# Kernel tuning notes

Measured on AMD Instinct MI355X. Metric: run time of the kernel, lower is better.

The kernel has to match this reference:

```python
import jax, jax.numpy as jnp
import numpy as np

N = 20000
E = 320000
F_IN = 256
NHID = 64
H1 = 8
H2 = 1
NUM_CLASSES = 40
NEG_SLOPE = 0.2


def setup_inputs() -> dict:
    key = jax.random.key(0)
    ks = jax.random.split(key, 11)
    glorot = lambda k, shape: jax.random.normal(k, shape, jnp.float32) * jnp.sqrt(2.0 / (shape[0] + shape[-1]))
    x = jax.random.normal(ks[0], (N, F_IN), jnp.float32)
    edge_index = jax.random.randint(ks[1], (2, E), 0, N, jnp.int64)
    W1 = glorot(ks[2], (F_IN, H1 * NHID))
    att_src1 = glorot(ks[3], (H1, NHID))
    att_dst1 = glorot(ks[4], (H1, NHID))
    b1 = jnp.zeros((H1 * NHID,), jnp.float32)
    W2 = glorot(ks[5], (H1 * NHID, H2 * NUM_CLASSES))
    att_src2 = glorot(ks[6], (H2, NUM_CLASSES))
    att_dst2 = glorot(ks[7], (H2, NUM_CLASSES))
    b2 = jnp.zeros((NUM_CLASSES,), jnp.float32)
    return {"x": x, "edge_index": edge_index, "W1": W1, "att_src1": att_src1,
            "att_dst1": att_dst1, "b1": b1, "W2": W2, "att_src2": att_src2,
            "att_dst2": att_dst2, "b2": b2}


def gat_conv(x, src, dst, W, a_src, a_dst, bias, concat):
    # x: [N, F_in], src/dst: [E'] (self-loops already appended)
    H, C = a_src.shape
    h = (x @ W).reshape(N, H, C)                       # [N,H,C]
    alpha_src = jnp.sum(h * a_src, axis=-1)            # [N,H]
    alpha_dst = jnp.sum(h * a_dst, axis=-1)            # [N,H]
    e = jax.nn.leaky_relu(alpha_src[src] + alpha_dst[dst], NEG_SLOPE)  # [E',H]
    # segment softmax over incoming edges of each dst node
    emax = jax.lax.stop_gradient(jax.ops.segment_max(e, dst, num_segments=N))
    ee = jnp.exp(e - emax[dst])
    denom = jax.ops.segment_sum(ee, dst, num_segments=N)
    alpha = ee / (denom[dst] + 1e-16)                  # [E',H]
    out = jax.ops.segment_sum(alpha[:, :, None] * h[src], dst, num_segments=N)  # [N,H,C]
    out = out.reshape(N, H * C) if concat else out.mean(axis=1)
    return out + bias


def reference(x, edge_index, W1, att_src1, att_dst1, b1, W2, att_src2, att_dst2, b2):
    # PyG GATConv adds self-loops by default
    loops = jnp.arange(N, dtype=edge_index.dtype)
    src = jnp.concatenate([edge_index[0], loops])
    dst = jnp.concatenate([edge_index[1], loops])
    h = gat_conv(x, src, dst, W1, att_src1, att_dst1, b1, concat=True)   # [N, H1*NHID]
    h = jax.nn.elu(h)
    out = gat_conv(h, src, dst, W2, att_src2, att_dst2, b2, concat=False)  # [N, NUM_CLASSES]
    return jax.nn.log_softmax(out, axis=1)
```

## Files before the change

kernel.cpp:

```cpp
#include <hip/hip_runtime.h>
#include <hip/hip_bf16.h>
#include <math.h>

#define N_NODES 20000
#define MPAD 20096
#define N_EDGES 320000
#define EP (N_EDGES + N_NODES)
#define F_IN 256
#define NHID 64
#define H1 8
#define D1 512
#define NCLS 40
#define NEG_SLOPE 0.2f
#define MAXD 128

typedef __attribute__((ext_vector_type(8))) short bf16x8;
typedef __attribute__((ext_vector_type(4))) float f32x4;

__device__ __forceinline__ float wave_max(float v) {
#pragma unroll
  for (int o = 32; o > 0; o >>= 1) v = fmaxf(v, __shfl_xor(v, o));
  return v;
}
__device__ __forceinline__ float wave_sum(float v) {
#pragma unroll
  for (int o = 32; o > 0; o >>= 1) v += __shfl_xor(v, o);
  return v;
}
__device__ __forceinline__ float bf2f(unsigned short u) {
  union { unsigned int i; float f; } c; c.i = ((unsigned int)u) << 16; return c.f;
}
__device__ __forceinline__ unsigned short f2bf(float f) {
  union { float f; unsigned int i; } c; c.f = f;
  unsigned int x = c.i;
  return (unsigned short)((x + 0x7fffu + ((x >> 16) & 1u)) >> 16);
}
__device__ __forceinline__ float asf(unsigned int u) {
  union { unsigned int i; float f; } c; c.i = u; return c.f;
}
__device__ __forceinline__ float lrelu(float x) { return x > 0.f ? x : NEG_SLOPE * x; }

__device__ __forceinline__ void gload16(const void* g, void* l) {
  __builtin_amdgcn_global_load_lds((const __attribute__((address_space(1))) void*)g,
                                   (__attribute__((address_space(3))) void*)l, 16, 0, 0);
}

#define PB_CONV 2512
#define PB_TW1  (PB_CONV + 32)
#define PB_TW2  (PB_TW1 + 96)
#define PB_ZERO (PB_TW2 + 157)
#define PB_PAD  (PB_ZERO + 24)
__global__ __launch_bounds__(256) void prep_kernel(const float* __restrict__ x,
                                                   const float* __restrict__ W1,
                                                   const float* __restrict__ W2,
                                                   unsigned short* __restrict__ xb,
                                                   unsigned short* __restrict__ wb1t,
                                                   unsigned short* __restrict__ wb2t,
                                                   int* __restrict__ deg,
                                                   int* __restrict__ cursor,
                                                   unsigned short* __restrict__ out1b) {
  __shared__ float tsh[64][65];
  int bid = blockIdx.x;
  int t = threadIdx.x;
  if (bid < PB_CONV) {
    size_t base = ((size_t)bid * 256 + t) * 8;
    int row = (int)(base >> 8);
    ushort4 o0, o1;
    if (row < N_NODES) {
      float4 v0 = *(const float4*)&x[base];
      float4 v1 = *(const float4*)&x[base + 4];
      o0 = make_ushort4(f2bf(v0.x), f2bf(v0.y), f2bf(v0.z), f2bf(v0.w));
      o1 = make_ushort4(f2bf(v1.x), f2bf(v1.y), f2bf(v1.z), f2bf(v1.w));
    } else {
      o0 = make_ushort4(0, 0, 0, 0); o1 = o0;
    }
    *(ushort4*)&xb[base] = o0;
    *(ushort4*)&xb[base + 4] = o1;
  } else if (bid < PB_TW1) {
    int b2 = bid - PB_CONV;
    int bk = b2 & 3, bn = b2 >> 2;
    int tr = t >> 4, tc4 = (t & 15) * 4;
#pragma unroll
    for (int i = 0; i < 4; ++i) {
      int k = i * 16 + tr;
      float4 v = *(const float4*)&W1[(size_t)(bk * 64 + k) * D1 + bn * 64 + tc4];
      tsh[k][tc4] = v.x; tsh[k][tc4 + 1] = v.y; tsh[k][tc4 + 2] = v.z; tsh[k][tc4 + 3] = v.w;
    }
    __syncthreads();
#pragma unroll
    for (int i = 0; i < 4; ++i) {
      int n = i * 16 + tr;
      ushort4 o = make_ushort4(f2bf(tsh[tc4][n]), f2bf(tsh[tc4 + 1][n]),
                               f2bf(tsh[tc4 + 2][n]), f2bf(tsh[tc4 + 3][n]));
      *(ushort4*)&wb1t[(size_t)(bn * 64 + n) * F_IN + bk * 64 + tc4] = o;
    }
  } else if (bid < PB_TW2) {
    int idx = (bid - PB_TW1) * 256 + t;
    int c = idx >> 9, k = idx & 511;
    wb2t[idx] = f2bf((c < NCLS) ? W2[(size_t)k * NCLS + c] : 0.f);
  } else if (bid < PB_ZERO) {
    int idx = (bid - PB_TW2) * 256 + t;
    if (idx < N_NODES) deg[idx] = 0;
    else if (idx < 2 * N_NODES) cursor[idx - N_NODES] = 0;
  } else {
    int idx = (bid - PB_ZERO) * 256 + t;
    uint4 z = make_uint4(0, 0, 0, 0);
    *(uint4*)((char*)out1b + (size_t)N_NODES * D1 * 2 + (size_t)idx * 16) = z;
  }
}

__global__ void count_deg(const int* __restrict__ ei, int* __restrict__ deg) {
  int e = blockIdx.x * blockDim.x + threadIdx.x;
  if (e >= EP) return;
  int dst = (e < N_EDGES) ? ei[N_EDGES + e] : (e - N_EDGES);
  atomicAdd(&deg[dst], 1);
}

#define SCAN_T 1024
#define SCAN_CHUNK 20
__global__ __launch_bounds__(1024) void scan_kernel(const int* __restrict__ deg,
                                                    int* __restrict__ offsets) {
  __shared__ int wsum[16];
  int t = threadIdx.x;
  int w = t >> 6, lane = t & 63;
  int lo = t * SCAN_CHUNK;
  int hi = min(lo + SCAN_CHUNK, N_NODES);
  int s = 0;
  for (int i = lo; i < hi; ++i) s += deg[i];
  int incl = s;
#pragma unroll
  for (int o = 1; o < 64; o <<= 1) {
    int v = __shfl_up(incl, o);
    if (lane >= o) incl += v;
  }
  if (lane == 63) wsum[w] = incl;
  __syncthreads();
  if (t == 0) {
    int run = 0;
#pragma unroll
    for (int i = 0; i < 16; ++i) { int v = wsum[i]; wsum[i] = run; run += v; }
  }
  __syncthreads();
  int off = wsum[w] + incl - s;
  for (int i = lo; i < hi; ++i) { offsets[i] = off; off += deg[i]; }
  if (hi == N_NODES && lo < N_NODES) offsets[N_NODES] = off;
}

__global__ void scatter_edges(const int* __restrict__ ei, const int* __restrict__ offsets,
                              int* __restrict__ cursor, int* __restrict__ edge_src) {
  int e = blockIdx.x * blockDim.x + threadIdx.x;
  if (e >= EP) return;
  int src, dst;
  if (e < N_EDGES) { src = ei[e]; dst = ei[N_EDGES + e]; }
  else             { src = dst = e - N_EDGES; }
  int pos = offsets[dst] + atomicAdd(&cursor[dst], 1);
  edge_src[pos] = src;
}

__global__ __launch_bounds__(256) void gemm1_mfma(const unsigned short* __restrict__ xb,
                                                  const unsigned short* __restrict__ wb1t,
                                                  const float* __restrict__ a_src,
                                                  const float* __restrict__ a_dst,
                                                  unsigned short* __restrict__ h1b,
                                                  float* __restrict__ asrc,
                                                  float* __restrict__ adst) {
  __shared__ unsigned short As[128 * 64];
  __shared__ unsigned short Bs[128 * 64];
  int tid = threadIdx.x;
  int w = tid >> 6, lane = tid & 63;
  int bn = blockIdx.x & 3, bm = blockIdx.x >> 2;
  int row0 = bm * 128, col0 = bn * 128;
  int wr = w >> 1, wc = w & 1;
  int cl = lane & 15, hi = lane >> 4;
  f32x4 acc[4][4] = {};
  for (int k0 = 0; k0 < F_IN; k0 += 64) {
#pragma unroll
    for (int c = 0; c < 4; ++c) {
      int slot = c * 256 + tid;
      int r = slot >> 3;
      int q = (slot & 7) ^ (r & 7);
      gload16(xb + (size_t)(row0 + r) * F_IN + k0 + q * 8, (char*)As + (c * 256 + w * 64) * 16);
      gload16(wb1t + (size_t)(col0 + r) * F_IN + k0 + q * 8, (char*)Bs + (c * 256 + w * 64) * 16);
    }
    __syncthreads();
#pragma unroll
    for (int kk = 0; kk < 2; ++kk) {
      bf16x8 a[4], b[4];
#pragma unroll
      for (int m = 0; m < 4; ++m) {
        int r = wr * 64 + m * 16 + cl;
        a[m] = *(const bf16x8*)&As[r * 64 + ((((kk * 4 + hi)) ^ (r & 7)) << 3)];
      }
#pragma unroll
      for (int n = 0; n < 4; ++n) {
        int r = wc * 64 + n * 16 + cl;
        b[n] = *(const bf16x8*)&Bs[r * 64 + ((((kk * 4 + hi)) ^ (r & 7)) << 3)];
      }
#pragma unroll
      for (int m = 0; m < 4; ++m)
#pragma unroll
        for (int n = 0; n < 4; ++n)
          acc[m][n] = __builtin_amdgcn_mfma_f32_16x16x32_bf16(a[m], b[n], acc[m][n], 0, 0, 0);
    }
    __syncthreads();
  }
  int head = bn * 2 + wc;
  float asv[4], adv[4];
#pragma unroll
  for (int n = 0; n < 4; ++n) {
    asv[n] = a_src[head * 64 + n * 16 + cl];
    adv[n] = a_dst[head * 64 + n * 16 + cl];
  }
#pragma unroll
  for (int m = 0; m < 4; ++m) {
#pragma unroll
    for (int r = 0; r < 4; ++r) {
      int grow = row0 + wr * 64 + m * 16 + hi * 4 + r;
      float ps = acc[m][0][r] * asv[0] + acc[m][1][r] * asv[1] +
                 acc[m][2][r] * asv[2] + acc[m][3][r] * asv[3];
      float pd = acc[m][0][r] * adv[0] + acc[m][1][r] * adv[1] +
                 acc[m][2][r] * adv[2] + acc[m][3][r] * adv[3];
#pragma unroll
      for (int o = 8; o > 0; o >>= 1) { ps += __shfl_xor(ps, o); pd += __shfl_xor(pd, o); }
      if (grow < N_NODES) {
#pragma unroll
        for (int n = 0; n < 4; ++n)
          h1b[(size_t)grow * D1 + col0 + wc * 64 + n * 16 + cl] = f2bf(acc[m][n][r]);
        if (cl == 0) { asrc[grow * H1 + head] = ps; adst[grow * H1 + head] = pd; }
      }
    }
  }
}

__global__ __launch_bounds__(128) void agg1_kernel(const int* __restrict__ offsets,
                                                   const int* __restrict__ edge_src,
                                                   const float* __restrict__ asrc,
                                                   const float* __restrict__ adst,
                                                   const unsigned short* __restrict__ h1b,
                                                   const float* __restrict__ b1,
                                                   unsigned short* __restrict__ out1b) {
  __shared__ float alphaT[MAXD][H1 + 1];
  __shared__ int   lsoff[MAXD];
  __shared__ float red[2][8];
  __shared__ float minv[2][8];
  __shared__ float accs[2][D1];
  int n = blockIdx.x;
  int t = threadIdx.x;
  int w = t >> 6, lane = t & 63;
  int base = offsets[n];
  int deg = offsets[n + 1] - base;
  int degc = min(deg, MAXD);

  for (int e = t; e < degc; e += 128) lsoff[e] = edge_src[base + e] << 10;
  __syncthreads();

  int h = t & 7;
  int et = t >> 3;
  float advv = adst[n * H1 + h];
  float m = -INFINITY;
  for (int e = et; e < degc; e += 16) {
    int s = lsoff[e] >> 10;
    float ev = lrelu(asrc[s * H1 + h] + advv);
    alphaT[e][h] = ev;
    m = fmaxf(m, ev);
  }
  for (int e = MAXD + et; e < deg; e += 16)
    m = fmaxf(m, lrelu(asrc[edge_src[base + e] * H1 + h] + advv));
  m = fmaxf(m, __shfl_xor(m, 8));
  m = fmaxf(m, __shfl_xor(m, 16));
  m = fmaxf(m, __shfl_xor(m, 32));
  if (lane < 8) red[w][lane] = m;
  __syncthreads();
  m = fmaxf(red[0][h], red[1][h]);
  float ss = 0.f;
  for (int e = et; e < degc; e += 16) ss += __expf(alphaT[e][h] - m);
  for (int e = MAXD + et; e < deg; e += 16)
    ss += __expf(lrelu(asrc[edge_src[base + e] * H1 + h] + advv) - m);
  ss += __shfl_xor(ss, 8);
  ss += __shfl_xor(ss, 16);
  ss += __shfl_xor(ss, 32);
  __syncthreads();
  if (lane < 8) red[w][lane] = ss;
  __syncthreads();
  float inv = 1.f / (red[0][h] + red[1][h] + 1e-16f);
  if (t < 8) { minv[0][t] = m; minv[1][t] = inv; }
  for (int e = et; e < degc; e += 16)
    alphaT[e][h] = __expf(alphaT[e][h] - m) * inv;
  __syncthreads();

  int myh = lane >> 3;
  const char* hb = (const char*)h1b + lane * 16;
  float acc[8] = {};
  int e = w;
  for (; e + 2 < degc; e += 4) {
    float a0 = alphaT[e][myh];
    float a1 = alphaT[e + 2][myh];
    uint4 u0 = *(const uint4*)(hb + lsoff[e]);
    uint4 u1 = *(const uint4*)(hb + lsoff[e + 2]);
#pragma unroll
    for (int j = 0; j < 4; ++j) {
      unsigned int x0 = ((const unsigned int*)&u0)[j];
      unsigned int x1 = ((const unsigned int*)&u1)[j];
      acc[2 * j]     += a0 * asf(x0 << 16);
      acc[2 * j + 1] += a0 * asf(x0 & 0xffff0000u);
      acc[2 * j]     += a1 * asf(x1 << 16);
      acc[2 * j + 1] += a1 * asf(x1 & 0xffff0000u);
    }
  }
  for (; e < degc; e += 2) {
    float a = alphaT[e][myh];
    uint4 uv = *(const uint4*)(hb + lsoff[e]);
#pragma unroll
    for (int j = 0; j < 4; ++j) {
      unsigned int u = ((const unsigned int*)&uv)[j];
      acc[2 * j]     += a * asf(u << 16);
      acc[2 * j + 1] += a * asf(u & 0xffff0000u);
    }
  }
  if (deg > MAXD) {
    float mh = minv[0][myh], invh = minv[1][myh];
    float advh = adst[n * H1 + myh];
    for (int e2 = MAXD + w; e2 < deg; e2 += 2) {
      int s = edge_src[base + e2];
      float a = __expf(lrelu(asrc[s * H1 + myh] + advh) - mh) * invh;
      uint4 uv = *(const uint4*)(hb + ((size_t)s << 10));
#pragma unroll
      for (int j = 0; j < 4; ++j) {
        unsigned int u = ((const unsigned int*)&uv)[j];
        acc[2 * j]     += a * asf(u << 16);
        acc[2 * j + 1] += a * asf(u & 0xffff0000u);
      }
    }
  }
  *(float4*)&accs[w][lane * 8]     = make_float4(acc[0], acc[1], acc[2], acc[3]);
  *(float4*)&accs[w][lane * 8 + 4] = make_float4(acc[4], acc[5], acc[6], acc[7]);
  __syncthreads();

  int c0 = t * 4;
  float4 s0 = *(float4*)&accs[0][c0];
  float4 s1 = *(float4*)&accs[1][c0];
  float4 bv = *(const float4*)&b1[c0];
  float v0 = s0.x + s1.x + bv.x, v1 = s0.y + s1.y + bv.y;
  float v2 = s0.z + s1.z + bv.z, v3 = s0.w + s1.w + bv.w;
  v0 = v0 > 0.f ? v0 : (__expf(v0) - 1.f);
  v1 = v1 > 0.f ? v1 : (__expf(v1) - 1.f);
  v2 = v2 > 0.f ? v2 : (__expf(v2) - 1.f);
  v3 = v3 > 0.f ? v3 : (__expf(v3) - 1.f);
  ushort4 o = make_ushort4(f2bf(v0), f2bf(v1), f2bf(v2), f2bf(v3));
  *(ushort4*)&out1b[(size_t)n * D1 + c0] = o;
}

__global__ __launch_bounds__(256) void gemm2_mfma(const unsigned short* __restrict__ ab,
                                                  const unsigned short* __restrict__ wb2t,
                                                  const float* __restrict__ a_src2,
                                                  const float* __restrict__ a_dst2,
                                                  float* __restrict__ h2,
                                                  float* __restrict__ asrc,
                                                  float* __restrict__ adst) {
  __shared__ unsigned short As[64 * 64];
  __shared__ unsigned short Bs[48 * 64];
  int tid = threadIdx.x;
  int w = tid >> 6, lane = tid & 63;
  int row0 = blockIdx.x * 64;
  int cl = lane & 15, hi = lane >> 4;
  f32x4 acc[3] = {};
  for (int k0 = 0; k0 < D1; k0 += 64) {
#pragma unroll
    for (int c = 0; c < 2; ++c) {
      int slot = c * 256 + tid;
      int r = slot >> 3;
      int q = (slot & 7) ^ (r & 7);
      gload16(ab + (size_t)(row0 + r) * D1 + k0 + q * 8, (char*)As + (c * 256 + w * 64) * 16);
    }
    {
      int r = tid >> 3;
      int q = (tid & 7) ^ (r & 7);
      gload16(wb2t + (size_t)r * D1 + k0 + q * 8, (char*)Bs + (w * 64) * 16);
      if (tid < 128) {
        int slot2 = 256 + tid;
        int r2 = slot2 >> 3;
        int q2 = (slot2 & 7) ^ (r2 & 7);
        gload16(wb2t + (size_t)r2 * D1 + k0 + q2 * 8, (char*)Bs + ((256 + w * 64)) * 16);
      }
    }
    __syncthreads();
#pragma unroll
    for (int kk = 0; kk < 2; ++kk) {
      int ra = w * 16 + cl;
      bf16x8 a = *(const bf16x8*)&As[ra * 64 + (((kk * 4 + hi) ^ (ra & 7)) << 3)];
#pragma unroll
      for (int n = 0; n < 3; ++n) {
        int rb = n * 16 + cl;
        bf16x8 b = *(const bf16x8*)&Bs[rb * 64 + (((kk * 4 + hi) ^ (rb & 7)) << 3)];
        acc[n] = __builtin_amdgcn_mfma_f32_16x16x32_bf16(a, b, acc[n], 0, 0, 0);
      }
    }
    __syncthreads();
  }
  float asv[3], adv[3];
#pragma unroll
  for (int n = 0; n < 3; ++n) {
    int c = n * 16 + cl;
    asv[n] = (c < NCLS) ? a_src2[c] : 0.f;
    adv[n] = (c < NCLS) ? a_dst2[c] : 0.f;
  }
#pragma unroll
  for (int r = 0; r < 4; ++r) {
    int grow = row0 + w * 16 + hi * 4 + r;
    float ps = acc[0][r] * asv[0] + acc[1][r] * asv[1] + acc[2][r] * asv[2];
    float pd = acc[0][r] * adv[0] + acc[1][r] * adv[1] + acc[2][r] * adv[2];
#pragma unroll
    for (int o = 8; o > 0; o >>= 1) { ps += __shfl_xor(ps, o); pd += __shfl_xor(pd, o); }
    if (grow < N_NODES) {
#pragma unroll
      for (int n = 0; n < 3; ++n) {
        int c = n * 16 + cl;
        if (c < NCLS) h2[(size_t)grow * NCLS + c] = acc[n][r];
      }
      if (cl == 0) { asrc[grow] = ps; adst[grow] = pd; }
    }
  }
}

__global__ __launch_bounds__(256) void agg2_kernel(const int* __restrict__ offsets,
                                                   const int* __restrict__ edge_src,
                                                   const float* __restrict__ asrc,
                                                   const float* __restrict__ adst,
                                                   const float* __restrict__ h2,
                                                   const float* __restrict__ b2,
                                                   float* __restrict__ out) {
  __shared__ float lalpha[4][MAXD];
  __shared__ int   lsoff[4][MAXD];
  int w = threadIdx.x >> 6;
  int lane = threadIdx.x & 63;
  int n = blockIdx.x * 4 + w;
  int base = offsets[n];
  int deg = offsets[n + 1] - base;
  int degc = min(deg, MAXD);
  int degp = ((degc + 2) / 3) * 3;

  float advv = adst[n];
  float m = -INFINITY;
  for (int e = lane; e < deg; e += 64) {
    int s = edge_src[base + e];
    float ev = lrelu(asrc[s] + advv);
    if (e < MAXD) { lsoff[w][e] = s * (NCLS * 4); lalpha[w][e] = ev; }
    m = fmaxf(m, ev);
  }
  m = wave_max(m);
  float ssum = 0.f;
  for (int e = lane; e < deg; e += 64) {
    float ev;
    if (e < MAXD) ev = lalpha[w][e];
    else { int s = edge_src[base + e]; ev = lrelu(asrc[s] + advv); }
    ssum += __expf(ev - m);
  }
  float inv = 1.f / (wave_sum(ssum) + 1e-16f);
  for (int e = lane; e < degc; e += 64) lalpha[w][e] = __expf(lalpha[w][e] - m) * inv;
  {
    int e = degc + lane;
    if (e < degp && e < MAXD) { lalpha[w][e] = 0.f; lsoff[w][e] = 0; }
  }

  int esub = lane / 20;
  int cg = lane - esub * 20;
  bool act = esub < 3;
  float ax = 0.f, ay = 0.f;
  const char* hb = (const char*)h2 + cg * 8;
  for (int i = 0; i < degp; i += 3) {
    if (act) {
      int slot = i + esub;
      float a = lalpha[w][slot];
      int so = lsoff[w][slot];
      float2 hv = *(const float2*)(hb + so);
      ax += a * hv.x; ay += a * hv.y;
    }
  }
  for (int e = MAXD + esub; e < deg; e += 3) {
    if (act) {
      int s = edge_src[base + e];
      float a = __expf(lrelu(asrc[s] + advv) - m) * inv;
      float2 hv = *(const float2*)(hb + (size_t)s * (NCLS * 4));
      ax += a * hv.x; ay += a * hv.y;
    }
  }
  float ax1 = __shfl(ax, lane + 20), ax2 = __shfl(ax, lane + 40);
  float ay1 = __shfl(ay, lane + 20), ay2 = __shfl(ay, lane + 40);
  float v0 = -INFINITY, v1 = -INFINITY;
  if (lane < 20) {
    v0 = ax + ax1 + ax2 + b2[2 * cg];
    v1 = ay + ay1 + ay2 + b2[2 * cg + 1];
  }
  float m2 = wave_max(fmaxf(v0, v1));
  float se = wave_sum(lane < 20 ? __expf(v0 - m2) + __expf(v1 - m2) : 0.f);
  if (lane < 20) {
    float ls = logf(se);
    *(float2*)&out[(size_t)n * NCLS + 2 * cg] = make_float2(v0 - m2 - ls, v1 - m2 - ls);
  }
}

extern "C" void kernel_launch(void* const* d_in, const int* in_sizes, int n_in,
                              void* d_out, int out_size, void* d_ws, size_t ws_size,
                              hipStream_t stream) {
  const float* x   = (const float*)d_in[0];
  const int*   ei  = (const int*)d_in[1];
  const float* W1  = (const float*)d_in[2];
  const float* as1 = (const float*)d_in[3];
  const float* ad1 = (const float*)d_in[4];
  const float* b1  = (const float*)d_in[5];
  const float* W2  = (const float*)d_in[6];
  const float* as2 = (const float*)d_in[7];
  const float* ad2 = (const float*)d_in[8];
  const float* b2  = (const float*)d_in[9];
  float* out = (float*)d_out;

  char* ws = (char*)d_ws;
  size_t off = 0;
  auto alloc = [&](size_t bytes) -> char* {
    char* p = ws + off;
    off += (bytes + 255) & ~(size_t)255;
    return p;
  };
  int* deg      = (int*)alloc((size_t)N_NODES * 4);
  int* cursor   = (int*)alloc((size_t)N_NODES * 4);
  int* offsets  = (int*)alloc((size_t)(N_NODES + 1) * 4);
  int* edge_src = (int*)alloc((size_t)EP * 4);
  unsigned short* xb    = (unsigned short*)alloc((size_t)MPAD * F_IN * 2);
  unsigned short* wb1t  = (unsigned short*)alloc((size_t)D1 * F_IN * 2);
  unsigned short* wb2t  = (unsigned short*)alloc((size_t)48 * D1 * 2);
  unsigned short* h1b   = (unsigned short*)alloc((size_t)N_NODES * D1 * 2);
  unsigned short* out1b = (unsigned short*)alloc((size_t)MPAD * D1 * 2);
  float* asrc1  = (float*)alloc((size_t)N_NODES * H1 * 4);
  float* adst1  = (float*)alloc((size_t)N_NODES * H1 * 4);
  float* h2     = (float*)alloc((size_t)N_NODES * NCLS * 4);
  float* asrc2  = (float*)alloc((size_t)N_NODES * 4);
  float* adst2  = (float*)alloc((size_t)N_NODES * 4);

  prep_kernel<<<PB_PAD, 256, 0, stream>>>(x, W1, W2, xb, wb1t, wb2t, deg, cursor, out1b);
  count_deg<<<(EP + 255) / 256, 256, 0, stream>>>(ei, deg);
  scan_kernel<<<1, SCAN_T, 0, stream>>>(deg, offsets);
  scatter_edges<<<(EP + 255) / 256, 256, 0, stream>>>(ei, offsets, cursor, edge_src);

  gemm1_mfma<<<157 * 4, 256, 0, stream>>>(xb, wb1t, as1, ad1, h1b, asrc1, adst1);
  agg1_kernel<<<N_NODES, 128, 0, stream>>>(offsets, edge_src, asrc1, adst1, h1b, b1, out1b);

  gemm2_mfma<<<MPAD / 64, 256, 0, stream>>>(out1b, wb2t, as2, ad2, h2, asrc2, adst2);
  agg2_kernel<<<N_NODES / 4, 256, 0, stream>>>(offsets, edge_src, asrc2, adst2, h2, b2, out);
}
```

Baseline: 159.3 us.

## Map one wavefront per destination node in layer-1 aggregation

The layer-1 aggregation kernel now runs four nodes per 256-thread block, one wavefront each, instead of one node per 128-thread block split across two waves. Block-level barriers and shared-memory reductions are replaced with wave barriers and shuffles, and the final cross-wave accumulator sum through LDS is gone. The intent is to remove synchronisation and reduction overhead and launch fewer blocks. In exchange, each wave walks the full edge list alone, so per-node latency rises and high-degree nodes may cause imbalance within a block. A wave barrier is also added in the layer-2 aggregation kernel.

```diff
diff --git a/kernel.cpp b/kernel.cpp
--- a/kernel.cpp
+++ b/kernel.cpp
@@ -232,71 +232,59 @@
   }
 }
 
-__global__ __launch_bounds__(128) void agg1_kernel(const int* __restrict__ offsets,
+__global__ __launch_bounds__(256) void agg1_kernel(const int* __restrict__ offsets,
                                                    const int* __restrict__ edge_src,
                                                    const float* __restrict__ asrc,
                                                    const float* __restrict__ adst,
                                                    const unsigned short* __restrict__ h1b,
                                                    const float* __restrict__ b1,
                                                    unsigned short* __restrict__ out1b) {
-  __shared__ float alphaT[MAXD][H1 + 1];
-  __shared__ int   lsoff[MAXD];
-  __shared__ float red[2][8];
-  __shared__ float minv[2][8];
-  __shared__ float accs[2][D1];
-  int n = blockIdx.x;
-  int t = threadIdx.x;
-  int w = t >> 6, lane = t & 63;
+  __shared__ float alphaT[4][MAXD][H1];
+  __shared__ int   lsoff[4][MAXD];
+  int w = threadIdx.x >> 6, lane = threadIdx.x & 63;
+  int n = blockIdx.x * 4 + w;
   int base = offsets[n];
   int deg = offsets[n + 1] - base;
   int degc = min(deg, MAXD);
 
-  for (int e = t; e < degc; e += 128) lsoff[e] = edge_src[base + e] << 10;
-  __syncthreads();
-
-  int h = t & 7;
-  int et = t >> 3;
+  for (int e = lane; e < degc; e += 64) lsoff[w][e] = edge_src[base + e] << 10;
+  __builtin_amdgcn_wave_barrier();
+
+  int h = lane & 7, et = lane >> 3;
   float advv = adst[n * H1 + h];
   float m = -INFINITY;
-  for (int e = et; e < degc; e += 16) {
-    int s = lsoff[e] >> 10;
+  for (int e = et; e < degc; e += 8) {
+    int s = lsoff[w][e] >> 10;
     float ev = lrelu(asrc[s * H1 + h] + advv);
-    alphaT[e][h] = ev;
+    alphaT[w][e][h] = ev;
     m = fmaxf(m, ev);
   }
-  for (int e = MAXD + et; e < deg; e += 16)
+  for (int e = MAXD + et; e < deg; e += 8)
     m = fmaxf(m, lrelu(asrc[edge_src[base + e] * H1 + h] + advv));
   m = fmaxf(m, __shfl_xor(m, 8));
   m = fmaxf(m, __shfl_xor(m, 16));
   m = fmaxf(m, __shfl_xor(m, 32));
-  if (lane < 8) red[w][lane] = m;
-  __syncthreads();
-  m = fmaxf(red[0][h], red[1][h]);
   float ss = 0.f;
-  for (int e = et; e < degc; e += 16) ss += __expf(alphaT[e][h] - m);
-  for (int e = MAXD + et; e < deg; e += 16)
+  for (int e = et; e < degc; e += 8) ss += __expf(alphaT[w][e][h] - m);
+  for (int e = MAXD + et; e < deg; e += 8)
     ss += __expf(lrelu(asrc[edge_src[base + e] * H1 + h] + advv) - m);
   ss += __shfl_xor(ss, 8);
   ss += __shfl_xor(ss, 16);
   ss += __shfl_xor(ss, 32);
-  __syncthreads();
-  if (lane < 8) red[w][lane] = ss;
-  __syncthreads();
-  float inv = 1.f / (red[0][h] + red[1][h] + 1e-16f);
-  if (t < 8) { minv[0][t] = m; minv[1][t] = inv; }
-  for (int e = et; e < degc; e += 16)
-    alphaT[e][h] = __expf(alphaT[e][h] - m) * inv;
-  __syncthreads();
+  float inv = 1.f / (ss + 1e-16f);
+  for (int e = et; e < degc; e += 8)
+    alphaT[w][e][h] = __expf(alphaT[w][e][h] - m) * inv;
+  __builtin_amdgcn_wave_barrier();
 
   int myh = lane >> 3;
   const char* hb = (const char*)h1b + lane * 16;
   float acc[8] = {};
-  int e = w;
-  for (; e + 2 < degc; e += 4) {
-    float a0 = alphaT[e][myh];
-    float a1 = alphaT[e + 2][myh];
-    uint4 u0 = *(const uint4*)(hb + lsoff[e]);
-    uint4 u1 = *(const uint4*)(hb + lsoff[e + 2]);
+  int e = 0;
+  for (; e + 1 < degc; e += 2) {
+    float a0 = alphaT[w][e][myh];
+    float a1 = alphaT[w][e + 1][myh];
+    uint4 u0 = *(const uint4*)(hb + lsoff[w][e]);
+    uint4 u1 = *(const uint4*)(hb + lsoff[w][e + 1]);
 #pragma unroll
     for (int j = 0; j < 4; ++j) {
       unsigned int x0 = ((const unsigned int*)&u0)[j];
@@ -307,9 +295,9 @@
       acc[2 * j + 1] += a1 * asf(x1 & 0xffff0000u);
     }
   }
-  for (; e < degc; e += 2) {
-    float a = alphaT[e][myh];
-    uint4 uv = *(const uint4*)(hb + lsoff[e]);
+  for (; e < degc; ++e) {
+    float a = alphaT[w][e][myh];
+    uint4 uv = *(const uint4*)(hb + lsoff[w][e]);
 #pragma unroll
     for (int j = 0; j < 4; ++j) {
       unsigned int u = ((const unsigned int*)&uv)[j];
@@ -318,9 +306,10 @@
     }
   }
   if (deg > MAXD) {
-    float mh = minv[0][myh], invh = minv[1][myh];
+    float mh = __shfl(m, myh);
+    float invh = __shfl(inv, myh);
     float advh = adst[n * H1 + myh];
-    for (int e2 = MAXD + w; e2 < deg; e2 += 2) {
+    for (int e2 = MAXD; e2 < deg; ++e2) {
       int s = edge_src[base + e2];
       float a = __expf(lrelu(asrc[s * H1 + myh] + advh) - mh) * invh;
       uint4 uv = *(const uint4*)(hb + ((size_t)s << 10));
@@ -332,22 +321,19 @@
       }
     }
   }
-  *(float4*)&accs[w][lane * 8]     = make_float4(acc[0], acc[1], acc[2], acc[3]);
-  *(float4*)&accs[w][lane * 8 + 4] = make_float4(acc[4], acc[5], acc[6], acc[7]);
-  __syncthreads();
-
-  int c0 = t * 4;
-  float4 s0 = *(float4*)&accs[0][c0];
-  float4 s1 = *(float4*)&accs[1][c0];
-  float4 bv = *(const float4*)&b1[c0];
-  float v0 = s0.x + s1.x + bv.x, v1 = s0.y + s1.y + bv.y;
-  float v2 = s0.z + s1.z + bv.z, v3 = s0.w + s1.w + bv.w;
-  v0 = v0 > 0.f ? v0 : (__expf(v0) - 1.f);
-  v1 = v1 > 0.f ? v1 : (__expf(v1) - 1.f);
-  v2 = v2 > 0.f ? v2 : (__expf(v2) - 1.f);
-  v3 = v3 > 0.f ? v3 : (__expf(v3) - 1.f);
-  ushort4 o = make_ushort4(f2bf(v0), f2bf(v1), f2bf(v2), f2bf(v3));
-  *(ushort4*)&out1b[(size_t)n * D1 + c0] = o;
+
+  int c0 = lane * 8;
+  float4 b0 = *(const float4*)&b1[c0];
+  float4 b4 = *(const float4*)&b1[c0 + 4];
+  float v[8];
+  v[0] = acc[0] + b0.x; v[1] = acc[1] + b0.y; v[2] = acc[2] + b0.z; v[3] = acc[3] + b0.w;
+  v[4] = acc[4] + b4.x; v[5] = acc[5] + b4.y; v[6] = acc[6] + b4.z; v[7] = acc[7] + b4.w;
+#pragma unroll
+  for (int j = 0; j < 8; ++j) v[j] = v[j] > 0.f ? v[j] : (__expf(v[j]) - 1.f);
+  ushort4 o0 = make_ushort4(f2bf(v[0]), f2bf(v[1]), f2bf(v[2]), f2bf(v[3]));
+  ushort4 o1 = make_ushort4(f2bf(v[4]), f2bf(v[5]), f2bf(v[6]), f2bf(v[7]));
+  *(ushort4*)&out1b[(size_t)n * D1 + c0] = o0;
+  *(ushort4*)&out1b[(size_t)n * D1 + c0 + 4] = o1;
 }
 
 __global__ __launch_bounds__(256) void gemm2_mfma(const unsigned short* __restrict__ ab,
@@ -461,6 +447,7 @@
     int e = degc + lane;
     if (e < degp && e < MAXD) { lalpha[w][e] = 0.f; lsoff[w][e] = 0; }
   }
+  __builtin_amdgcn_wave_barrier();
 
   int esub = lane / 20;
   int cg = lane - esub * 20;
@@ -542,7 +529,7 @@
   scatter_edges<<<(EP + 255) / 256, 256, 0, stream>>>(ei, offsets, cursor, edge_src);
 
   gemm1_mfma<<<157 * 4, 256, 0, stream>>>(xb, wb1t, as1, ad1, h1b, asrc1, adst1);
-  agg1_kernel<<<N_NODES, 128, 0, stream>>>(offsets, edge_src, asrc1, adst1, h1b, b1, out1b);
+  agg1_kernel<<<N_NODES / 4, 256, 0, stream>>>(offsets, edge_src, asrc1, adst1, h1b, b1, out1b);
 
   gemm2_mfma<<<MPAD / 64, 256, 0, stream>>>(out1b, wb2t, as2, ad2, h2, asrc2, adst2);
   agg2_kernel<<<N_NODES / 4, 256, 0, stream>>>(offsets, edge_src, asrc2, adst2, h2, b2, out);
```

New measurement: 159.3 us. About the same (+0.0%).
